# Optimization experiments

Hardware: AMD Instinct MI355X
Metric: run time of the kernel (lower is better)

## Reference

```python
import jax, jax.numpy as jnp
import numpy as np

N = 100000
E = 3200000
IN_F = 128
OUT_F = 64
ALPHA = 0.1  # leaky relu negative slope


def spmm(rows, cols, vals, X):
    # sparse [N,N] (COO) @ dense [N,F] -> [N,F]
    return jax.ops.segment_sum(vals[:, None] * X[cols], rows, num_segments=N)


def setup_inputs() -> dict:
    key = jax.random.key(0)
    ks = jax.random.split(key, 16)
    d = {
        "x": jax.random.normal(ks[0], (N, IN_F), dtype=jnp.float32),
        "W": jax.random.normal(ks[1], (IN_F, OUT_F), dtype=jnp.float32) * (1.414 / np.sqrt(IN_F)),
        "a": jax.random.normal(ks[2], (2 * OUT_F, 1), dtype=jnp.float32) * 0.1,
    }
    names = ["A", "P1", "P2", "P3"]
    for i, nm in enumerate(names):
        d[nm + "_rows"] = jax.random.randint(ks[3 + 3 * i], (E,), 0, N, dtype=jnp.int32)
        d[nm + "_cols"] = jax.random.randint(ks[4 + 3 * i], (E,), 0, N, dtype=jnp.int32)
        d[nm + "_vals"] = jax.random.uniform(ks[5 + 3 * i], (E,), dtype=jnp.float32) / 32.0
    return d


def reference(x, W, a, A_rows, A_cols, A_vals,
              P1_rows, P1_cols, P1_vals,
              P2_rows, P2_cols, P2_vals,
              P3_rows, P3_cols, P3_vals):
    support0 = x @ W                         # [N, F]
    h_A = spmm(A_rows, A_cols, A_vals, support0)
    h_A2 = spmm(A_rows, A_cols, A_vals, h_A)
    h_A3 = spmm(A_rows, A_cols, A_vals, h_A2)
    h_sct1 = jnp.abs(spmm(P1_rows, P1_cols, P1_vals, support0))
    h_sct2 = jnp.abs(spmm(P2_rows, P2_cols, P2_vals, support0))
    h_sct3 = jnp.abs(spmm(P3_rows, P3_cols, P3_vals, support0))

    h = support0
    F2 = 2 * OUT_F
    # faithful to torch: cat along dim0 then raw row-major view(N, 1, 2F)
    def pair(hk):
        return jnp.concatenate([h, hk], axis=0).reshape(N, 1, F2)

    a_input = jnp.concatenate(
        [pair(h_A), pair(h_A2), pair(h_A3), pair(h_sct1), pair(h_sct2), pair(h_sct3)],
        axis=1,
    ).reshape(N, 6, F2)
    e = jax.nn.leaky_relu((a_input @ a)[..., 0], negative_slope=ALPHA)  # [N, 6]
    attention = jax.nn.softmax(e, axis=1).reshape(N, 6, 1)
    # faithful to torch: cat along dim2 -> [N,F,6], then raw view(N,6,F)
    h_all = jnp.stack([h_A, h_A2, h_A3, h_sct1, h_sct2, h_sct3], axis=2).reshape(N, 6, OUT_F)
    h_prime = jnp.mean(attention * h_all, axis=1)  # [N, F]
    return (h_prime, attention)
```

## Files before the change

### kernel.cpp

```cpp
#include <hip/hip_runtime.h>
#include <math.h>

#define NN 100000
#define EE 3200000
#define INF 128
#define OUTF 64
#define ALPHA 0.1f

#define BROWS 128
#define NBINS 782
#define CAP 4472
#define SCHUNK 4096
#define NCH 4
#define SBLK (SCHUNK * NCH)
#define NSUM ((NBINS + 3) / 4)

#define GR 64
#define XPAD 132

__device__ __forceinline__ unsigned short f2bf(float f)
{
    unsigned u = __float_as_uint(f);
    u += 0x7FFFu + ((u >> 16) & 1u);
    return (unsigned short)(u >> 16);
}
__device__ __forceinline__ float bf2f(unsigned short b)
{
    return __uint_as_float((unsigned)b << 16);
}

__global__ __launch_bounds__(256) void gemm_kernel(
    const float* __restrict__ x, const float* __restrict__ W,
    unsigned short* __restrict__ outbf)
{
    __shared__ float Wl[INF * OUTF];
    __shared__ float xL[GR * XPAD];

    int tid = threadIdx.x;
    int tx = tid & 15;
    int ty = tid >> 4;
    int r0 = blockIdx.x * GR;

    const float4* W4 = (const float4*)W;
    float4* Wl4 = (float4*)Wl;
    for (int i = tid; i < INF * OUTF / 4; i += 256) Wl4[i] = W4[i];

    for (int i = tid; i < GR * (INF / 4); i += 256) {
        int row = i >> 5;
        int c4 = i & 31;
        int gr = r0 + row;
        float4 v = make_float4(0.f, 0.f, 0.f, 0.f);
        if (gr < NN) v = *(const float4*)&x[(size_t)gr * INF + 4 * c4];
        *(float4*)&xL[row * XPAD + 4 * c4] = v;
    }
    __syncthreads();

    float acc[4][4];
#pragma unroll
    for (int i = 0; i < 4; i++)
#pragma unroll
        for (int j = 0; j < 4; j++) acc[i][j] = 0.f;

#pragma unroll 4
    for (int k4 = 0; k4 < INF / 4; k4++) {
        float4 xv[4], wv[4];
#pragma unroll
        for (int i = 0; i < 4; i++)
            xv[i] = *(float4*)&xL[(4 * ty + i) * XPAD + 4 * k4];
#pragma unroll
        for (int kk = 0; kk < 4; kk++)
            wv[kk] = *(float4*)&Wl[(4 * k4 + kk) * OUTF + 4 * tx];
#pragma unroll
        for (int i = 0; i < 4; i++) {
#pragma unroll
            for (int kk = 0; kk < 4; kk++) {
                acc[i][0] = fmaf(((float*)&xv[i])[kk], ((float*)&wv[kk])[0], acc[i][0]);
                acc[i][1] = fmaf(((float*)&xv[i])[kk], ((float*)&wv[kk])[1], acc[i][1]);
                acc[i][2] = fmaf(((float*)&xv[i])[kk], ((float*)&wv[kk])[2], acc[i][2]);
                acc[i][3] = fmaf(((float*)&xv[i])[kk], ((float*)&wv[kk])[3], acc[i][3]);
            }
        }
    }

#pragma unroll
    for (int i = 0; i < 4; i++) {
        int gr = r0 + 4 * ty + i;
        if (gr < NN) {
            uint2 o;
            o.x = (unsigned)f2bf(acc[i][0]) | ((unsigned)f2bf(acc[i][1]) << 16);
            o.y = (unsigned)f2bf(acc[i][2]) | ((unsigned)f2bf(acc[i][3]) << 16);
            *(uint2*)&outbf[(size_t)gr * OUTF + 4 * tx] = o;
        }
    }
}

__global__ __launch_bounds__(256) void bin_scatter4(
    const int* __restrict__ rows0, const int* __restrict__ cols0, const float* __restrict__ vals0,
    const int* __restrict__ rows1, const int* __restrict__ cols1, const float* __restrict__ vals1,
    const int* __restrict__ rows2, const int* __restrict__ cols2, const float* __restrict__ vals2,
    const int* __restrict__ rows3, const int* __restrict__ cols3, const float* __restrict__ vals3,
    int* __restrict__ gcur_all,
    uint2* __restrict__ b0, uint2* __restrict__ b1,
    uint2* __restrict__ b2, uint2* __restrict__ b3)
{
    __shared__ uint2 rec[SCHUNK];
    __shared__ unsigned short bin_of[SCHUNK];
    __shared__ int hc[NCH][NBINS];
    __shared__ int lcur[NBINS];
    __shared__ int off[NBINS + 1];
    __shared__ int cur[NBINS];
    __shared__ int sums[NSUM];

    int m = blockIdx.y;
    const int* rows; const int* cols; const float* vals; uint2* binned;
    if (m == 0)      { rows = rows0; cols = cols0; vals = vals0; binned = b0; }
    else if (m == 1) { rows = rows1; cols = cols1; vals = vals1; binned = b1; }
    else if (m == 2) { rows = rows2; cols = cols2; vals = vals2; binned = b2; }
    else             { rows = rows3; cols = cols3; vals = vals3; binned = b3; }
    int* gcur = gcur_all + m * NBINS;

    int tid = threadIdx.x;
    int base = blockIdx.x * SBLK;
    int n = min(SBLK, EE - base);
    if (n <= 0) return;

    for (int i = tid; i < NCH * NBINS; i += 256) ((int*)hc)[i] = 0;
    __syncthreads();
    for (int i = tid; i < n; i += 256) {
        int r = rows[base + i];
        atomicAdd(&hc[i >> 12][r >> 7], 1);
    }
    __syncthreads();
    for (int b = tid; b < NBINS; b += 256) {
        int c = hc[0][b] + hc[1][b] + hc[2][b] + hc[3][b];
        lcur[b] = c ? atomicAdd(&gcur[b], c) : 0;
    }

    for (int cc = 0; cc < NCH; cc++) {
        int c0 = cc * SCHUNK;
        if (c0 >= n) break;
        int nc = min(SCHUNK, n - c0);
        __syncthreads();
        if (tid < NSUM) {
            int s = 0;
#pragma unroll
            for (int k = 0; k < 4; k++) { int b = 4 * tid + k; if (b < NBINS) s += hc[cc][b]; }
            sums[tid] = s;
        }
        __syncthreads();
        if (tid == 0) {
            int acc = 0;
            for (int t = 0; t < NSUM; t++) { int v = sums[t]; sums[t] = acc; acc += v; }
            off[NBINS] = acc;
        }
        __syncthreads();
        if (tid < NSUM) {
            int acc = sums[tid];
#pragma unroll
            for (int k = 0; k < 4; k++) {
                int b = 4 * tid + k;
                if (b < NBINS) { off[b] = acc; cur[b] = acc; acc += hc[cc][b]; }
            }
        }
        __syncthreads();
        for (int i = tid; i < nc; i += 256) {
            int r = rows[base + c0 + i];
            int ccol = cols[base + c0 + i];
            float v = vals[base + c0 + i];
            int b = r >> 7;
            int pos = atomicAdd(&cur[b], 1);
            uint2 q;
            q.x = (unsigned)ccol | ((unsigned)(r & (BROWS - 1)) << 17);
            q.y = __float_as_uint(v);
            rec[pos] = q;
            bin_of[pos] = (unsigned short)b;
        }
        __syncthreads();
        for (int i = tid; i < nc; i += 256) {
            int b = bin_of[i];
            int slot = lcur[b] + (i - off[b]);
            if (slot < CAP) binned[(size_t)b * CAP + slot] = rec[i];
        }
        __syncthreads();
        for (int b = tid; b < NBINS; b += 256) lcur[b] += hc[cc][b];
    }
}

__global__ __launch_bounds__(256) void bin_sort4(
    uint2* __restrict__ b0, uint2* __restrict__ b1,
    uint2* __restrict__ b2, uint2* __restrict__ b3,
    const int* __restrict__ gcur_all,
    int* __restrict__ rowptr_all, int* __restrict__ cnt_all)
{
    __shared__ uint2 rin[CAP];
    __shared__ uint2 rout[CAP];
    __shared__ int h[BROWS], hs[BROWS], cur[BROWS];

    int m = blockIdx.y;
    uint2* binned = (m == 0) ? b0 : (m == 1) ? b1 : (m == 2) ? b2 : b3;
    const int* gcur = gcur_all + m * NBINS;
    int* rowptr = rowptr_all + m * NN;
    int* cnt = cnt_all + m * NN;

    int bin = blockIdx.x;
    int tid = threadIdx.x;
    int c = min(gcur[bin], CAP);
    uint2* src = binned + (size_t)bin * CAP;

    for (int i = tid; i < c; i += 256) rin[i] = src[i];
    if (tid < BROWS) h[tid] = 0;
    __syncthreads();
    for (int i = tid; i < c; i += 256)
        atomicAdd(&h[(rin[i].x >> 17) & (BROWS - 1)], 1);
    __syncthreads();
    if (tid < BROWS) hs[tid] = h[tid];
    __syncthreads();
#pragma unroll
    for (int o = 1; o < BROWS; o <<= 1) {
        int w = (tid >= o && tid < BROWS) ? hs[tid - o] : 0;
        __syncthreads();
        if (tid < BROWS) hs[tid] += w;
        __syncthreads();
    }
    if (tid < BROWS) cur[tid] = hs[tid] - h[tid];
    __syncthreads();
    for (int i = tid; i < c; i += 256) {
        uint2 q = rin[i];
        int pos = atomicAdd(&cur[(q.x >> 17) & (BROWS - 1)], 1);
        rout[pos] = q;
    }
    __syncthreads();
    for (int i = tid; i < c; i += 256) src[i] = rout[i];

    if (tid < BROWS) {
        int gr = bin * BROWS + tid;
        if (gr < NN) {
            rowptr[gr] = bin * CAP + (hs[tid] - h[tid]);
            cnt[gr] = h[tid];
        }
    }
}

__device__ __forceinline__ void spmm_row(
    const int* __restrict__ rowptr, const int* __restrict__ cnt,
    const uint2* __restrict__ edges,
    const unsigned short* __restrict__ Xb, unsigned short* __restrict__ Yb)
{
    int row = blockIdx.x * 4 + (threadIdx.x >> 6);
    int lane = threadIdx.x & 63;
    if (row >= NN) return;
    int s = __builtin_amdgcn_readfirstlane(rowptr[row]);
    int e = s + __builtin_amdgcn_readfirstlane(cnt[row]);
    float acc = 0.f;
    int i = s;
    for (; i + 7 < e; i += 8) {
        uint2 p0 = edges[i + 0], p1 = edges[i + 1], p2 = edges[i + 2], p3 = edges[i + 3];
        uint2 p4 = edges[i + 4], p5 = edges[i + 5], p6 = edges[i + 6], p7 = edges[i + 7];
        unsigned short x0 = Xb[(size_t)(p0.x & 0x1FFFF) * OUTF + lane];
        unsigned short x1 = Xb[(size_t)(p1.x & 0x1FFFF) * OUTF + lane];
        unsigned short x2 = Xb[(size_t)(p2.x & 0x1FFFF) * OUTF + lane];
        unsigned short x3 = Xb[(size_t)(p3.x & 0x1FFFF) * OUTF + lane];
        unsigned short x4 = Xb[(size_t)(p4.x & 0x1FFFF) * OUTF + lane];
        unsigned short x5 = Xb[(size_t)(p5.x & 0x1FFFF) * OUTF + lane];
        unsigned short x6 = Xb[(size_t)(p6.x & 0x1FFFF) * OUTF + lane];
        unsigned short x7 = Xb[(size_t)(p7.x & 0x1FFFF) * OUTF + lane];
        acc = fmaf(__uint_as_float(p0.y), bf2f(x0), acc);
        acc = fmaf(__uint_as_float(p1.y), bf2f(x1), acc);
        acc = fmaf(__uint_as_float(p2.y), bf2f(x2), acc);
        acc = fmaf(__uint_as_float(p3.y), bf2f(x3), acc);
        acc = fmaf(__uint_as_float(p4.y), bf2f(x4), acc);
        acc = fmaf(__uint_as_float(p5.y), bf2f(x5), acc);
        acc = fmaf(__uint_as_float(p6.y), bf2f(x6), acc);
        acc = fmaf(__uint_as_float(p7.y), bf2f(x7), acc);
    }
    for (; i < e; i++) {
        uint2 p = edges[i];
        acc = fmaf(__uint_as_float(p.y),
                   bf2f(Xb[(size_t)(p.x & 0x1FFFF) * OUTF + lane]), acc);
    }
    Yb[(size_t)row * OUTF + lane] = f2bf(acc);
}

__global__ __launch_bounds__(256) void spmm_csr(
    const int* __restrict__ rowptr, const int* __restrict__ cnt,
    const uint2* __restrict__ edges,
    const unsigned short* __restrict__ Xb, unsigned short* __restrict__ Yb)
{
    spmm_row(rowptr, cnt, edges, Xb, Yb);
}

__global__ __launch_bounds__(256) void spmm_p3(
    const int* __restrict__ rowptr_all, const int* __restrict__ cnt_all,
    const uint2* __restrict__ b1, const uint2* __restrict__ b2, const uint2* __restrict__ b3,
    const unsigned short* __restrict__ sup,
    unsigned short* __restrict__ s1, unsigned short* __restrict__ s2, unsigned short* __restrict__ s3)
{
    int m = blockIdx.y;
    const uint2* edges = (m == 0) ? b1 : (m == 1) ? b2 : b3;
    unsigned short* out = (m == 0) ? s1 : (m == 1) ? s2 : s3;
    spmm_row(rowptr_all + (m + 1) * NN, cnt_all + (m + 1) * NN, edges, sup, out);
}

__global__ __launch_bounds__(256) void fuse_kernel(
    const unsigned short* __restrict__ hA, const unsigned short* __restrict__ hA2,
    const unsigned short* __restrict__ hA3,
    const unsigned short* __restrict__ s1, const unsigned short* __restrict__ s2,
    const unsigned short* __restrict__ s3,
    const float* __restrict__ a, float* __restrict__ out)
{
    __shared__ float chl[4][6][OUTF];
    int wid = threadIdx.x >> 6;
    int lane = threadIdx.x & 63;
    int i = blockIdx.x * 4 + wid;
    if (i >= NN) return;

    const unsigned short* bufs[6] = {hA, hA2, hA3, s1, s2, s3};

#pragma unroll
    for (int k = 0; k < 6; k++) {
        float v = bf2f(bufs[k][(size_t)i * OUTF + lane]);
        if (k >= 3) v = fabsf(v);
        chl[wid][k][lane] = v;
    }

    float att[6];
    if (i < NN / 2) {
#pragma unroll
        for (int k = 0; k < 6; k++) att[k] = 1.0f / 6.0f;
    } else {
        int m = 2 * i - NN;
        float alo = a[lane];
        float ahi = a[64 + lane];
        float e[6];
#pragma unroll
        for (int k = 0; k < 6; k++) {
            float v0 = bf2f(bufs[k][(size_t)m * OUTF + lane]);
            float v1 = bf2f(bufs[k][(size_t)(m + 1) * OUTF + lane]);
            if (k >= 3) { v0 = fabsf(v0); v1 = fabsf(v1); }
            float p = alo * v0 + ahi * v1;
#pragma unroll
            for (int off = 32; off; off >>= 1) p += __shfl_xor(p, off);
            e[k] = (p > 0.f) ? p : ALPHA * p;
        }
        float mx = e[0];
#pragma unroll
        for (int k = 1; k < 6; k++) mx = fmaxf(mx, e[k]);
        float s = 0.f;
#pragma unroll
        for (int k = 0; k < 6; k++) { att[k] = __expf(e[k] - mx); s += att[k]; }
        float inv = 1.f / s;
#pragma unroll
        for (int k = 0; k < 6; k++) att[k] *= inv;
    }

    if (lane < 6) out[(size_t)NN * OUTF + (size_t)i * 6 + lane] = att[lane];

    float hp = 0.f;
#pragma unroll
    for (int j = 0; j < 6; j++) {
        int g = j * 64 + lane;
        hp += att[j] * chl[wid][g % 6][g / 6];
    }
    out[(size_t)i * OUTF + lane] = hp * (1.0f / 6.0f);
}

extern "C" void kernel_launch(void* const* d_in, const int* in_sizes, int n_in,
                              void* d_out, int out_size, void* d_ws, size_t ws_size,
                              hipStream_t stream)
{
    const float* x = (const float*)d_in[0];
    const float* W = (const float*)d_in[1];
    const float* a = (const float*)d_in[2];
    const int*   A_rows  = (const int*)d_in[3];
    const int*   A_cols  = (const int*)d_in[4];
    const float* A_vals  = (const float*)d_in[5];
    const int*   P1_rows = (const int*)d_in[6];
    const int*   P1_cols = (const int*)d_in[7];
    const float* P1_vals = (const float*)d_in[8];
    const int*   P2_rows = (const int*)d_in[9];
    const int*   P2_cols = (const int*)d_in[10];
    const float* P2_vals = (const float*)d_in[11];
    const int*   P3_rows = (const int*)d_in[12];
    const int*   P3_cols = (const int*)d_in[13];
    const float* P3_vals = (const float*)d_in[14];

    const size_t NF = (size_t)NN * OUTF;
    const size_t BINSZ = (size_t)NBINS * CAP;

    char* p = (char*)d_ws;
    uint2* b1 = (uint2*)p;              p += BINSZ * sizeof(uint2);
    uint2* b2 = (uint2*)p;              p += BINSZ * sizeof(uint2);
    uint2* b3 = (uint2*)p;              p += BINSZ * sizeof(uint2);
    unsigned short* bf_sup = (unsigned short*)p;  p += NF * 2;
    unsigned short* bf_hA  = (unsigned short*)p;  p += NF * 2;
    unsigned short* bf_hA2 = (unsigned short*)p;  p += NF * 2;
    unsigned short* bf_hA3 = (unsigned short*)p;  p += NF * 2;
    unsigned short* bf_s1  = (unsigned short*)p;  p += NF * 2;
    unsigned short* bf_s2  = (unsigned short*)p;  p += NF * 2;
    unsigned short* bf_s3  = (unsigned short*)p;  p += NF * 2;
    int* gcur   = (int*)p;              p += (size_t)4 * NBINS * sizeof(int);
    int* rowptr = (int*)p;              p += (size_t)4 * NN * sizeof(int);
    int* cnt    = (int*)p;              p += (size_t)4 * NN * sizeof(int);

    uint2* b0 = (uint2*)d_out;

    const int GB = (EE + SBLK - 1) / SBLK;
    const int RB = (NN + 3) / 4;

    hipMemsetAsync(gcur, 0, (size_t)4 * NBINS * sizeof(int), stream);

    gemm_kernel<<<(NN + GR - 1) / GR, 256, 0, stream>>>(x, W, bf_sup);

    bin_scatter4<<<dim3(GB, 4), 256, 0, stream>>>(
        A_rows, A_cols, A_vals, P1_rows, P1_cols, P1_vals,
        P2_rows, P2_cols, P2_vals, P3_rows, P3_cols, P3_vals,
        gcur, b0, b1, b2, b3);

    bin_sort4<<<dim3(NBINS, 4), 256, 0, stream>>>(b0, b1, b2, b3, gcur, rowptr, cnt);

    spmm_p3<<<dim3(RB, 3), 256, 0, stream>>>(rowptr, cnt, b1, b2, b3,
                                             bf_sup, bf_s1, bf_s2, bf_s3);

    spmm_csr<<<RB, 256, 0, stream>>>(rowptr, cnt, b0, bf_sup, bf_hA);
    spmm_csr<<<RB, 256, 0, stream>>>(rowptr, cnt, b0, bf_hA,  bf_hA2);
    spmm_csr<<<RB, 256, 0, stream>>>(rowptr, cnt, b0, bf_hA2, bf_hA3);

    fuse_kernel<<<RB, 256, 0, stream>>>(bf_hA, bf_hA2, bf_hA3,
                                        bf_s1, bf_s2, bf_s3, a, (float*)d_out);
}
```

Measured before the change: 773.9 us.

## Sort bin edges by column chunk and sweep SpMM per bin for gather locality

Each row bin is now sorted by a combined key of column chunk and local row, and a per-bin prefix table replaces the per-row CSR pointers. A new spmm_sweep kernel runs one block per bin and walks the column chunks in order, so the X gathers from all wavefronts fall in the same column range at once and reuse cache better. Each wave holds 16 row accumulators in registers. The scatter also drops the bin_of shared array by packing the low bits of the bin into the record and recovering the full bin from offsets, halves NCH, and reuses bf_sup as the hA3 buffer. In exchange the sweep loop adds data-dependent branching and lowers parallelism per row, and the sort adds a larger histogram plus a 256-entry scan.

```diff
diff --git a/kernel.cpp b/kernel.cpp
--- a/kernel.cpp
+++ b/kernel.cpp
@@ -11,9 +11,14 @@
 #define NBINS 782
 #define CAP 4472
 #define SCHUNK 4096
-#define NCH 4
+#define NCH 2
 #define SBLK (SCHUNK * NCH)
 #define NSUM ((NBINS + 3) / 4)
+
+#define CSHIFT 13
+#define NCHUNK 13
+#define NKEY 1664
+#define RCPS 1666
 
 #define GR 64
 #define XPAD 132
@@ -104,7 +109,6 @@
     uint2* __restrict__ b2, uint2* __restrict__ b3)
 {
     __shared__ uint2 rec[SCHUNK];
-    __shared__ unsigned short bin_of[SCHUNK];
     __shared__ int hc[NCH][NBINS];
     __shared__ int lcur[NBINS];
     __shared__ int off[NBINS + 1];
@@ -132,7 +136,7 @@
     }
     __syncthreads();
     for (int b = tid; b < NBINS; b += 256) {
-        int c = hc[0][b] + hc[1][b] + hc[2][b] + hc[3][b];
+        int c = hc[0][b] + hc[1][b];
         lcur[b] = c ? atomicAdd(&gcur[b], c) : 0;
     }
 
@@ -170,16 +174,20 @@
             int b = r >> 7;
             int pos = atomicAdd(&cur[b], 1);
             uint2 q;
-            q.x = (unsigned)ccol | ((unsigned)(r & (BROWS - 1)) << 17);
+            q.x = (unsigned)ccol | ((unsigned)(r & (BROWS - 1)) << 17)
+                | ((unsigned)(b & 0xFF) << 24);
             q.y = __float_as_uint(v);
             rec[pos] = q;
-            bin_of[pos] = (unsigned short)b;
         }
         __syncthreads();
         for (int i = tid; i < nc; i += 256) {
-            int b = bin_of[i];
+            uint2 q = rec[i];
+            int b = (int)(q.x >> 24);
+            if (b + 768 < NBINS && off[b + 768] <= i) b += 768;
+            else if (b + 512 < NBINS && off[b + 512] <= i) b += 512;
+            else if (b + 256 < NBINS && off[b + 256] <= i) b += 256;
             int slot = lcur[b] + (i - off[b]);
-            if (slot < CAP) binned[(size_t)b * CAP + slot] = rec[i];
+            if (slot < CAP) binned[(size_t)b * CAP + slot] = q;
         }
         __syncthreads();
         for (int b = tid; b < NBINS; b += 256) lcur[b] += hc[cc][b];
@@ -189,116 +197,101 @@
 __global__ __launch_bounds__(256) void bin_sort4(
     uint2* __restrict__ b0, uint2* __restrict__ b1,
     uint2* __restrict__ b2, uint2* __restrict__ b3,
-    const int* __restrict__ gcur_all,
-    int* __restrict__ rowptr_all, int* __restrict__ cnt_all)
-{
-    __shared__ uint2 rin[CAP];
+    const int* __restrict__ gcur_all, unsigned short* __restrict__ rcp_all)
+{
     __shared__ uint2 rout[CAP];
-    __shared__ int h[BROWS], hs[BROWS], cur[BROWS];
+    __shared__ int h[2048];
+    __shared__ int cur[2048];
+    __shared__ int part[256];
 
     int m = blockIdx.y;
     uint2* binned = (m == 0) ? b0 : (m == 1) ? b1 : (m == 2) ? b2 : b3;
     const int* gcur = gcur_all + m * NBINS;
-    int* rowptr = rowptr_all + m * NN;
-    int* cnt = cnt_all + m * NN;
-
     int bin = blockIdx.x;
     int tid = threadIdx.x;
+    unsigned short* rcp = rcp_all + ((size_t)m * NBINS + bin) * RCPS;
+
     int c = min(gcur[bin], CAP);
     uint2* src = binned + (size_t)bin * CAP;
 
-    for (int i = tid; i < c; i += 256) rin[i] = src[i];
-    if (tid < BROWS) h[tid] = 0;
-    __syncthreads();
-    for (int i = tid; i < c; i += 256)
-        atomicAdd(&h[(rin[i].x >> 17) & (BROWS - 1)], 1);
-    __syncthreads();
-    if (tid < BROWS) hs[tid] = h[tid];
-    __syncthreads();
-#pragma unroll
-    for (int o = 1; o < BROWS; o <<= 1) {
-        int w = (tid >= o && tid < BROWS) ? hs[tid - o] : 0;
-        __syncthreads();
-        if (tid < BROWS) hs[tid] += w;
-        __syncthreads();
-    }
-    if (tid < BROWS) cur[tid] = hs[tid] - h[tid];
+    for (int k = tid; k < 2048; k += 256) h[k] = 0;
     __syncthreads();
     for (int i = tid; i < c; i += 256) {
-        uint2 q = rin[i];
-        int pos = atomicAdd(&cur[(q.x >> 17) & (BROWS - 1)], 1);
+        uint2 q = src[i];
+        int key = (((q.x & 0x1FFFF) >> CSHIFT) << 7) | ((q.x >> 17) & 127);
+        atomicAdd(&h[key], 1);
+    }
+    __syncthreads();
+    int b0i = tid * 8, s = 0;
+#pragma unroll
+    for (int k = 0; k < 8; k++) s += h[b0i + k];
+    part[tid] = s;
+    __syncthreads();
+    for (int o = 1; o < 256; o <<= 1) {
+        int w = (tid >= o) ? part[tid - o] : 0;
+        __syncthreads();
+        part[tid] += w;
+        __syncthreads();
+    }
+    int acc = part[tid] - s;
+#pragma unroll
+    for (int k = 0; k < 8; k++) {
+        int v = h[b0i + k];
+        h[b0i + k] = acc;
+        cur[b0i + k] = acc;
+        acc += v;
+    }
+    __syncthreads();
+    for (int i = tid; i < c; i += 256) {
+        uint2 q = src[i];
+        int key = (((q.x & 0x1FFFF) >> CSHIFT) << 7) | ((q.x >> 17) & 127);
+        int pos = atomicAdd(&cur[key], 1);
         rout[pos] = q;
     }
     __syncthreads();
     for (int i = tid; i < c; i += 256) src[i] = rout[i];
-
-    if (tid < BROWS) {
-        int gr = bin * BROWS + tid;
-        if (gr < NN) {
-            rowptr[gr] = bin * CAP + (hs[tid] - h[tid]);
-            cnt[gr] = h[tid];
-        }
-    }
-}
-
-__device__ __forceinline__ void spmm_row(
-    const int* __restrict__ rowptr, const int* __restrict__ cnt,
+    for (int k = tid; k <= NKEY; k += 256) rcp[k] = (unsigned short)h[k];
+}
+
+__global__ __launch_bounds__(512) void spmm_sweep(
+    const unsigned short* __restrict__ rcp_all,
     const uint2* __restrict__ edges,
-    const unsigned short* __restrict__ Xb, unsigned short* __restrict__ Yb)
-{
-    int row = blockIdx.x * 4 + (threadIdx.x >> 6);
+    const unsigned short* __restrict__ Xb,
+    unsigned short* __restrict__ Yb)
+{
+    int bin = blockIdx.x;
+    int w = threadIdx.x >> 6;
     int lane = threadIdx.x & 63;
-    if (row >= NN) return;
-    int s = __builtin_amdgcn_readfirstlane(rowptr[row]);
-    int e = s + __builtin_amdgcn_readfirstlane(cnt[row]);
-    float acc = 0.f;
-    int i = s;
-    for (; i + 7 < e; i += 8) {
-        uint2 p0 = edges[i + 0], p1 = edges[i + 1], p2 = edges[i + 2], p3 = edges[i + 3];
-        uint2 p4 = edges[i + 4], p5 = edges[i + 5], p6 = edges[i + 6], p7 = edges[i + 7];
-        unsigned short x0 = Xb[(size_t)(p0.x & 0x1FFFF) * OUTF + lane];
-        unsigned short x1 = Xb[(size_t)(p1.x & 0x1FFFF) * OUTF + lane];
-        unsigned short x2 = Xb[(size_t)(p2.x & 0x1FFFF) * OUTF + lane];
-        unsigned short x3 = Xb[(size_t)(p3.x & 0x1FFFF) * OUTF + lane];
-        unsigned short x4 = Xb[(size_t)(p4.x & 0x1FFFF) * OUTF + lane];
-        unsigned short x5 = Xb[(size_t)(p5.x & 0x1FFFF) * OUTF + lane];
-        unsigned short x6 = Xb[(size_t)(p6.x & 0x1FFFF) * OUTF + lane];
-        unsigned short x7 = Xb[(size_t)(p7.x & 0x1FFFF) * OUTF + lane];
-        acc = fmaf(__uint_as_float(p0.y), bf2f(x0), acc);
-        acc = fmaf(__uint_as_float(p1.y), bf2f(x1), acc);
-        acc = fmaf(__uint_as_float(p2.y), bf2f(x2), acc);
-        acc = fmaf(__uint_as_float(p3.y), bf2f(x3), acc);
-        acc = fmaf(__uint_as_float(p4.y), bf2f(x4), acc);
-        acc = fmaf(__uint_as_float(p5.y), bf2f(x5), acc);
-        acc = fmaf(__uint_as_float(p6.y), bf2f(x6), acc);
-        acc = fmaf(__uint_as_float(p7.y), bf2f(x7), acc);
-    }
-    for (; i < e; i++) {
-        uint2 p = edges[i];
-        acc = fmaf(__uint_as_float(p.y),
-                   bf2f(Xb[(size_t)(p.x & 0x1FFFF) * OUTF + lane]), acc);
-    }
-    Yb[(size_t)row * OUTF + lane] = f2bf(acc);
-}
-
-__global__ __launch_bounds__(256) void spmm_csr(
-    const int* __restrict__ rowptr, const int* __restrict__ cnt,
-    const uint2* __restrict__ edges,
-    const unsigned short* __restrict__ Xb, unsigned short* __restrict__ Yb)
-{
-    spmm_row(rowptr, cnt, edges, Xb, Yb);
-}
-
-__global__ __launch_bounds__(256) void spmm_p3(
-    const int* __restrict__ rowptr_all, const int* __restrict__ cnt_all,
-    const uint2* __restrict__ b1, const uint2* __restrict__ b2, const uint2* __restrict__ b3,
-    const unsigned short* __restrict__ sup,
-    unsigned short* __restrict__ s1, unsigned short* __restrict__ s2, unsigned short* __restrict__ s3)
-{
-    int m = blockIdx.y;
-    const uint2* edges = (m == 0) ? b1 : (m == 1) ? b2 : b3;
-    unsigned short* out = (m == 0) ? s1 : (m == 1) ? s2 : s3;
-    spmm_row(rowptr_all + (m + 1) * NN, cnt_all + (m + 1) * NN, edges, sup, out);
+    const unsigned short* pre = rcp_all + (size_t)bin * RCPS;
+    const uint2* eb = edges + (size_t)bin * CAP;
+
+    float acc[16];
+#pragma unroll
+    for (int r = 0; r < 16; r++) acc[r] = 0.f;
+
+    for (int cch = 0; cch < NCHUNK; cch++) {
+        int i = pre[(cch << 7) + (w << 4)];
+        int e = pre[(cch << 7) + (w << 4) + 16];
+#pragma unroll
+        for (int r = 0; r < 16; r++) {
+            float a = acc[r];
+            while (i < e) {
+                uint2 q = eb[i];
+                if ((int)((q.x >> 17) & 15) != r) break;
+                a = fmaf(__uint_as_float(q.y),
+                         bf2f(Xb[(size_t)(q.x & 0x1FFFF) * OUTF + lane]), a);
+                i++;
+            }
+            acc[r] = a;
+        }
+    }
+
+    int grow = bin * BROWS + w * 16;
+#pragma unroll
+    for (int r = 0; r < 16; r++) {
+        int gr = grow + r;
+        if (gr < NN) Yb[(size_t)gr * OUTF + lane] = f2bf(acc[r]);
+    }
 }
 
 __global__ __launch_bounds__(256) void fuse_kernel(
@@ -394,18 +387,17 @@
     unsigned short* bf_sup = (unsigned short*)p;  p += NF * 2;
     unsigned short* bf_hA  = (unsigned short*)p;  p += NF * 2;
     unsigned short* bf_hA2 = (unsigned short*)p;  p += NF * 2;
-    unsigned short* bf_hA3 = (unsigned short*)p;  p += NF * 2;
     unsigned short* bf_s1  = (unsigned short*)p;  p += NF * 2;
     unsigned short* bf_s2  = (unsigned short*)p;  p += NF * 2;
     unsigned short* bf_s3  = (unsigned short*)p;  p += NF * 2;
-    int* gcur   = (int*)p;              p += (size_t)4 * NBINS * sizeof(int);
-    int* rowptr = (int*)p;              p += (size_t)4 * NN * sizeof(int);
-    int* cnt    = (int*)p;              p += (size_t)4 * NN * sizeof(int);
+    unsigned short* rcp = (unsigned short*)p;     p += (size_t)4 * NBINS * RCPS * 2;
+    int* gcur = (int*)p;                p += (size_t)4 * NBINS * sizeof(int);
 
     uint2* b0 = (uint2*)d_out;
 
     const int GB = (EE + SBLK - 1) / SBLK;
     const int RB = (NN + 3) / 4;
+    const size_t RM = (size_t)NBINS * RCPS;
 
     hipMemsetAsync(gcur, 0, (size_t)4 * NBINS * sizeof(int), stream);
 
@@ -416,15 +408,15 @@
         P2_rows, P2_cols, P2_vals, P3_rows, P3_cols, P3_vals,
         gcur, b0, b1, b2, b3);
 
-    bin_sort4<<<dim3(NBINS, 4), 256, 0, stream>>>(b0, b1, b2, b3, gcur, rowptr, cnt);
-
-    spmm_p3<<<dim3(RB, 3), 256, 0, stream>>>(rowptr, cnt, b1, b2, b3,
-                                             bf_sup, bf_s1, bf_s2, bf_s3);
-
-    spmm_csr<<<RB, 256, 0, stream>>>(rowptr, cnt, b0, bf_sup, bf_hA);
-    spmm_csr<<<RB, 256, 0, stream>>>(rowptr, cnt, b0, bf_hA,  bf_hA2);
-    spmm_csr<<<RB, 256, 0, stream>>>(rowptr, cnt, b0, bf_hA2, bf_hA3);
-
-    fuse_kernel<<<RB, 256, 0, stream>>>(bf_hA, bf_hA2, bf_hA3,
+    bin_sort4<<<dim3(NBINS, 4), 256, 0, stream>>>(b0, b1, b2, b3, gcur, rcp);
+
+    spmm_sweep<<<NBINS, 512, 0, stream>>>(rcp + 1 * RM, b1, bf_sup, bf_s1);
+    spmm_sweep<<<NBINS, 512, 0, stream>>>(rcp + 2 * RM, b2, bf_sup, bf_s2);
+    spmm_sweep<<<NBINS, 512, 0, stream>>>(rcp + 3 * RM, b3, bf_sup, bf_s3);
+    spmm_sweep<<<NBINS, 512, 0, stream>>>(rcp + 0 * RM, b0, bf_sup, bf_hA);
+    spmm_sweep<<<NBINS, 512, 0, stream>>>(rcp + 0 * RM, b0, bf_hA, bf_hA2);
+    spmm_sweep<<<NBINS, 512, 0, stream>>>(rcp + 0 * RM, b0, bf_hA2, bf_sup);
+
+    fuse_kernel<<<RB, 256, 0, stream>>>(bf_hA, bf_hA2, bf_sup,
                                         bf_s1, bf_s2, bf_s3, a, (float*)d_out);
 }
```

Result: slower. 2.630 ms (+239.9%).
